# Performance work log

Measured on AMD Instinct MI355X. Metric: run time of the kernel, lower is better.

Reference implementation:

```python
import jax, jax.numpy as jnp
import numpy as np

NEG_SLOPE = 0.01  # torch F.leaky_relu default


def _gcn(x, W, b, src, dst, w, n_nodes):
    # PyG GCNConv(normalize=False, add_self_loops=False):
    # out[i] = sum_{e:(j->i)} w_e * (x @ W)[j] + b
    xw = x @ W                              # [N, out]
    msg = w[:, None] * xw[src]              # [E, out] gather
    return jax.ops.segment_sum(msg, dst, num_segments=n_nodes) + b


def setup_inputs() -> dict:
    key = jax.random.key(0)
    ks = jax.random.split(key, 12)
    N, E, B = 50000, 800000, 50
    d_in, d_hid, d_out = 128, 128, 128
    nodes_per_graph = N // B

    features = jax.random.normal(ks[0], (N, d_in), dtype=jnp.float32)
    adjs = jax.random.randint(ks[1], (2, E), 0, N, dtype=jnp.int32)
    values = jax.random.uniform(ks[2], (E,), dtype=jnp.float32)
    # root of graph g is its first node
    root_idx = jnp.arange(B, dtype=jnp.int32) * nodes_per_graph
    knowledge_node_num = jnp.full((B,), nodes_per_graph, dtype=jnp.int32)
    knowledge_edge_num = jnp.full((B,), E // B, dtype=jnp.int32)
    batch = jnp.arange(N, dtype=jnp.int32) // nodes_per_graph

    scale = 1.0 / np.sqrt(d_in)
    W1 = jax.random.uniform(ks[3], (d_in, d_hid), jnp.float32, -scale, scale)
    b1 = jax.random.uniform(ks[4], (d_hid,), jnp.float32, -scale, scale)
    W2 = jax.random.uniform(ks[5], (d_hid + d_in, d_out), jnp.float32, -scale, scale)
    b2 = jax.random.uniform(ks[6], (d_out,), jnp.float32, -scale, scale)
    Wl = jax.random.uniform(ks[7], (d_out + d_hid, d_in), jnp.float32, -scale, scale)
    bl = jax.random.uniform(ks[8], (d_in,), jnp.float32, -scale, scale)

    return {"features": features, "values": values, "W1": W1, "b1": b1,
            "W2": W2, "b2": b2, "Wl": Wl, "bl": bl,
            "adjs": adjs, "root_idx": root_idx,
            "knowledge_node_num": knowledge_node_num,
            "knowledge_edge_num": knowledge_edge_num, "batch": batch}


def reference(features, values, W1, b1, W2, b2, Wl, bl,
              adjs, root_idx, knowledge_node_num, knowledge_edge_num, batch):
    N = features.shape[0]
    B = knowledge_node_num.shape[0]
    src, dst = adjs[0], adjs[1]

    # per-node graph id (replaces the python loop building batch_k)
    batch_k = jnp.repeat(jnp.arange(B), knowledge_node_num, total_repeat_length=N)

    x0 = features                                    # features_1
    h1 = _gcn(x0, W1, b1, src, dst, values, N)       # conv1; features_2

    # root_extend: each node gets the raw features of its graph's root
    root1 = x0[root_idx[batch_k]]                    # [N, d_in]
    h = jax.nn.leaky_relu(jnp.concatenate([h1, root1], axis=1), NEG_SLOPE)
    # dropout=0.0 -> identity

    h2 = jax.nn.leaky_relu(_gcn(h, W2, b2, src, dst, values, N), NEG_SLOPE)

    root2 = h1[root_idx[batch_k]]                    # [N, d_hid] from conv1 output
    h = jnp.concatenate([h2, root2], axis=1)
    out = jax.nn.leaky_relu(h @ Wl + bl, NEG_SLOPE)
    return out
```

## Files before the change

kernel.cpp:

```cpp
#include <hip/hip_runtime.h>
#include <hip/hip_bf16.h>

#define NEG_SLOPE 0.01f
#define SCAN_CHUNK 1024

typedef __attribute__((ext_vector_type(8))) short short8;
typedef __attribute__((ext_vector_type(4))) float f32x4;

__device__ __forceinline__ float lrelu(float x) { return x > 0.f ? x : NEG_SLOPE * x; }

__device__ __forceinline__ unsigned short f2bf(float f) {
    unsigned u = __builtin_bit_cast(unsigned, f);
    u += 0x7fffu + ((u >> 16) & 1u);
    return (unsigned short)(u >> 16);
}
__device__ __forceinline__ float bf2f(unsigned short h) {
    return __builtin_bit_cast(float, (unsigned)h << 16);
}
__device__ __forceinline__ float bflo(unsigned u) {
    return __builtin_bit_cast(float, u << 16);
}
__device__ __forceinline__ float bfhi(unsigned u) {
    return __builtin_bit_cast(float, u & 0xffff0000u);
}

__global__ __launch_bounds__(256) void prep_kernel(
        const float* __restrict__ features, const int* __restrict__ batch,
        const int* __restrict__ root_idx, const float* __restrict__ W1,
        const float* __restrict__ W2, const float* __restrict__ Wl,
        unsigned short* __restrict__ feat16, int* __restrict__ rmap,
        int* __restrict__ deg, unsigned short* __restrict__ wt1,
        unsigned short* __restrict__ wt2, unsigned short* __restrict__ wtl, int N) {
    const int total = N * 32;
    for (int i = blockIdx.x * blockDim.x + threadIdx.x; i < total;
         i += gridDim.x * blockDim.x) {
        float4 v = *(const float4*)(features + (size_t)i * 4);
        ushort4 p;
        p.x = f2bf(v.x); p.y = f2bf(v.y); p.z = f2bf(v.z); p.w = f2bf(v.w);
        *(ushort4*)(feat16 + (size_t)i * 4) = p;
        if (i < N) { rmap[i] = root_idx[batch[i]]; deg[i] = 0; }
        if (i < 128 * 128) {
            int k = i >> 7, c = i & 127;
            wt1[c * 128 + k] = f2bf(W1[i]);
        }
        if (i < 256 * 128) {
            int k = i >> 7, c = i & 127;
            wt2[c * 256 + k] = f2bf(W2[i]);
            wtl[c * 256 + k] = f2bf(Wl[i]);
        }
    }
}

__global__ void count_kernel(const int* __restrict__ dst, int* __restrict__ deg, int E) {
    const int stride = gridDim.x * blockDim.x;
    const int i = blockIdx.x * blockDim.x + threadIdx.x;
    const int e4 = E >> 2;
    for (int q = i; q < e4; q += stride) {
        int4 d = ((const int4*)dst)[q];
        atomicAdd(&deg[d.x], 1);
        atomicAdd(&deg[d.y], 1);
        atomicAdd(&deg[d.z], 1);
        atomicAdd(&deg[d.w], 1);
    }
    for (int e = e4 * 4 + i; e < E; e += stride) atomicAdd(&deg[dst[e]], 1);
}

__global__ __launch_bounds__(256) void scan1_kernel(const int* __restrict__ deg,
                                                    int* __restrict__ rowstart,
                                                    int* __restrict__ chunksum, int N) {
    __shared__ int ts[256];
    const int b = blockIdx.x, t = threadIdx.x;
    const int base = b * SCAN_CHUNK + t * 4;
    int v[4], s = 0;
#pragma unroll
    for (int j = 0; j < 4; ++j) {
        v[j] = (base + j < N) ? deg[base + j] : 0;
        s += v[j];
    }
    ts[t] = s;
    __syncthreads();
    for (int off = 1; off < 256; off <<= 1) {
        int x = (t >= off) ? ts[t - off] : 0;
        __syncthreads();
        ts[t] += x;
        __syncthreads();
    }
    int run = ts[t] - s;
#pragma unroll
    for (int j = 0; j < 4; ++j) {
        if (base + j < N) rowstart[base + j] = run;
        run += v[j];
    }
    if (t == 255) chunksum[b] = ts[255];
}

__global__ void scan2_kernel(const int* __restrict__ chunksum, int* __restrict__ chunkoff,
                             int nchunks, int* __restrict__ rowstart, int N, int E) {
    if (blockIdx.x == 0 && threadIdx.x == 0) {
        int acc = 0;
        for (int i = 0; i < nchunks; ++i) { chunkoff[i] = acc; acc += chunksum[i]; }
        rowstart[N] = E;
    }
}

__global__ void scan3_kernel(int* __restrict__ rowstart, const int* __restrict__ chunkoff,
                             int* __restrict__ cursor, int N) {
    for (int i = blockIdx.x * blockDim.x + threadIdx.x; i < N; i += gridDim.x * blockDim.x) {
        int v = rowstart[i] + chunkoff[i / SCAN_CHUNK];
        rowstart[i] = v;
        cursor[i] = v;
    }
}

__global__ void fill_kernel(const int* __restrict__ src, const int* __restrict__ dst,
                            const float* __restrict__ vals, int* __restrict__ cursor,
                            int2* __restrict__ edata, int E) {
    const int stride = gridDim.x * blockDim.x;
    const int i = blockIdx.x * blockDim.x + threadIdx.x;
    const int e4 = E >> 2;
    for (int q = i; q < e4; q += stride) {
        int4 s = ((const int4*)src)[q];
        int4 d = ((const int4*)dst)[q];
        float4 v = ((const float4*)vals)[q];
        int p;
        p = atomicAdd(&cursor[d.x], 1);
        edata[p] = make_int2(s.x, __builtin_bit_cast(int, v.x));
        p = atomicAdd(&cursor[d.y], 1);
        edata[p] = make_int2(s.y, __builtin_bit_cast(int, v.y));
        p = atomicAdd(&cursor[d.z], 1);
        edata[p] = make_int2(s.z, __builtin_bit_cast(int, v.z));
        p = atomicAdd(&cursor[d.w], 1);
        edata[p] = make_int2(s.w, __builtin_bit_cast(int, v.w));
    }
    for (int e = e4 * 4 + i; e < E; e += stride) {
        int p = atomicAdd(&cursor[dst[e]], 1);
        edata[p] = make_int2(src[e], __builtin_bit_cast(int, vals[e]));
    }
}

__global__ __launch_bounds__(256) void gather_kernel(const unsigned short* __restrict__ xw,
                                                     const int* __restrict__ rowstart,
                                                     const int2* __restrict__ edata,
                                                     const float* __restrict__ bias,
                                                     unsigned short* __restrict__ h, int N) {
    const int node = blockIdx.x * 4 + (threadIdx.x >> 6);
    const int lane = threadIdx.x & 63;
    if (node >= N) return;
    const int s0 = rowstart[node], s1 = rowstart[node + 1];
    float2 acc = *(const float2*)(bias + lane * 2);
    int e = s0;
    for (; e + 4 <= s1; e += 4) {
        int2 e0 = edata[e], e1 = edata[e + 1], e2 = edata[e + 2], e3 = edata[e + 3];
        unsigned xa = *(const unsigned*)(xw + (size_t)e0.x * 128 + lane * 2);
        unsigned xb = *(const unsigned*)(xw + (size_t)e1.x * 128 + lane * 2);
        unsigned xc = *(const unsigned*)(xw + (size_t)e2.x * 128 + lane * 2);
        unsigned xd = *(const unsigned*)(xw + (size_t)e3.x * 128 + lane * 2);
        float va = __builtin_bit_cast(float, e0.y), vb = __builtin_bit_cast(float, e1.y);
        float vc = __builtin_bit_cast(float, e2.y), vd = __builtin_bit_cast(float, e3.y);
        acc.x = fmaf(va, bflo(xa), acc.x);
        acc.y = fmaf(va, bfhi(xa), acc.y);
        acc.x = fmaf(vb, bflo(xb), acc.x);
        acc.y = fmaf(vb, bfhi(xb), acc.y);
        acc.x = fmaf(vc, bflo(xc), acc.x);
        acc.y = fmaf(vc, bfhi(xc), acc.y);
        acc.x = fmaf(vd, bflo(xd), acc.x);
        acc.y = fmaf(vd, bfhi(xd), acc.y);
    }
    for (; e < s1; ++e) {
        int2 e0 = edata[e];
        float va = __builtin_bit_cast(float, e0.y);
        unsigned xa = *(const unsigned*)(xw + (size_t)e0.x * 128 + lane * 2);
        acc.x = fmaf(va, bflo(xa), acc.x);
        acc.y = fmaf(va, bfhi(xa), acc.y);
    }
    unsigned pk = (unsigned)f2bf(acc.x) | ((unsigned)f2bf(acc.y) << 16);
    *(unsigned*)(h + (size_t)node * 128 + lane * 2) = pk;
}

template <int K, bool LRA, bool LRB, bool LROUT, bool HASB, bool OUTBF>
__global__ __launch_bounds__(256) void mgemm_kernel(const unsigned short* __restrict__ A,
                                                    const unsigned short* __restrict__ B2,
                                                    const int* __restrict__ rmap,
                                                    const unsigned short* __restrict__ Wt,
                                                    const float* __restrict__ bias,
                                                    void* __restrict__ outv, int N) {
    __shared__ short As[64 * 32];
    __shared__ short Bs[128 * 32];
    const int tid = threadIdx.x;
    const int wv = tid >> 6, lane = tid & 63;
    const int lr = lane & 15, lg = lane >> 4;
    const int row0 = blockIdx.x * 64;

    const int arow = tid >> 2, apart = tid & 3;
    const int grow = row0 + arow;
    const int gr = grow < N ? grow : N - 1;
    const int rr = (K > 128) ? rmap[gr] : 0;
    const int bc = tid & 127, bhalf = (tid >> 7) * 16;

    f32x4 acc[8];
#pragma unroll
    for (int t = 0; t < 8; ++t) acc[t] = (f32x4){0.f, 0.f, 0.f, 0.f};

#pragma unroll 1
    for (int kc = 0; kc < K / 32; ++kc) {
        const int k0 = kc * 32;
        {
            const int kbase = k0 + apart * 8;
            const bool inA = kbase < 128;
            const unsigned short* sp = inA ? A + (size_t)gr * 128 + kbase
                                           : B2 + (size_t)rr * 128 + (kbase - 128);
            short8 v = *(const short8*)sp;
            const bool dolr = inA ? LRA : LRB;
            if (dolr) {
#pragma unroll
                for (int j = 0; j < 8; ++j)
                    v[j] = (short)f2bf(lrelu(bf2f((unsigned short)v[j])));
            }
            *(short8*)&As[arow * 32 + apart * 8] = v;
        }
        {
            const unsigned short* wsrc = Wt + (size_t)bc * K + k0 + bhalf;
            *(short8*)&Bs[bc * 32 + bhalf]     = *(const short8*)wsrc;
            *(short8*)&Bs[bc * 32 + bhalf + 8] = *(const short8*)(wsrc + 8);
        }
        __syncthreads();
        short8 af = *(short8*)&As[(wv * 16 + lr) * 32 + lg * 8];
#pragma unroll
        for (int t = 0; t < 8; ++t) {
            short8 bf = *(short8*)&Bs[(t * 16 + lr) * 32 + lg * 8];
            acc[t] = __builtin_amdgcn_mfma_f32_16x16x32_bf16(af, bf, acc[t], 0, 0, 0);
        }
        __syncthreads();
    }

#pragma unroll
    for (int t = 0; t < 8; ++t) {
#pragma unroll
        for (int r = 0; r < 4; ++r) {
            int grr = row0 + wv * 16 + lg * 4 + r;
            if (grr < N) {
                float v = acc[t][r];
                if (HASB) v += bias[t * 16 + lr];
                if (LROUT) v = lrelu(v);
                if (OUTBF)
                    ((unsigned short*)outv)[(size_t)grr * 128 + t * 16 + lr] = f2bf(v);
                else
                    ((float*)outv)[(size_t)grr * 128 + t * 16 + lr] = v;
            }
        }
    }
}

extern "C" void kernel_launch(void* const* d_in, const int* in_sizes, int n_in,
                              void* d_out, int out_size, void* d_ws, size_t ws_size,
                              hipStream_t stream) {
    const float* features = (const float*)d_in[0];
    const float* values   = (const float*)d_in[1];
    const float* W1 = (const float*)d_in[2];
    const float* b1 = (const float*)d_in[3];
    const float* W2 = (const float*)d_in[4];
    const float* b2 = (const float*)d_in[5];
    const float* Wl = (const float*)d_in[6];
    const float* bl = (const float*)d_in[7];
    const int* adjs     = (const int*)d_in[8];
    const int* root_idx = (const int*)d_in[9];
    const int* batch    = (const int*)d_in[12];
    float* out = (float*)d_out;

    const int N = in_sizes[0] / 128;
    const int E = in_sizes[1];
    const int* src = adjs;
    const int* dst = adjs + E;

    const size_t nf = (size_t)N * 128;
    unsigned short* bufA   = (unsigned short*)d_ws;
    unsigned short* h1     = bufA + nf;
    unsigned short* h2     = h1 + nf;
    unsigned short* feat16 = h2 + nf;
    unsigned short* wt1 = feat16 + nf;
    unsigned short* wt2 = wt1 + 128 * 128;
    unsigned short* wtl = wt2 + 256 * 128;
    uintptr_t ep = ((uintptr_t)(wtl + 256 * 128) + 7) & ~(uintptr_t)7;
    int2* edata    = (int2*)ep;
    int*  rmap     = (int*)(edata + E);
    int*  deg      = rmap + N;
    int*  rowstart = deg + N;
    int*  cursor   = rowstart + N + 1;
    int*  chunksum = cursor + N;
    int*  chunkoff = chunksum + 128;

    const int nchunks = (N + SCAN_CHUNK - 1) / SCAN_CHUNK;
    const int gblocks = (N + 63) / 64;

    prep_kernel<<<1024, 256, 0, stream>>>(features, batch, root_idx, W1, W2, Wl,
                                          feat16, rmap, deg, wt1, wt2, wtl, N);
    count_kernel<<<512, 256, 0, stream>>>(dst, deg, E);
    scan1_kernel<<<nchunks, 256, 0, stream>>>(deg, rowstart, chunksum, N);
    scan2_kernel<<<1, 64, 0, stream>>>(chunksum, chunkoff, nchunks, rowstart, N, E);
    scan3_kernel<<<64, 256, 0, stream>>>(rowstart, chunkoff, cursor, N);
    fill_kernel<<<512, 256, 0, stream>>>(src, dst, values, cursor, edata, E);

    mgemm_kernel<128, false, false, false, false, true>
        <<<gblocks, 256, 0, stream>>>(feat16, nullptr, nullptr, wt1, nullptr, bufA, N);
    gather_kernel<<<(N + 3) / 4, 256, 0, stream>>>(bufA, rowstart, edata, b1, h1, N);

    mgemm_kernel<256, true, true, false, false, true>
        <<<gblocks, 256, 0, stream>>>(h1, feat16, rmap, wt2, nullptr, bufA, N);
    gather_kernel<<<(N + 3) / 4, 256, 0, stream>>>(bufA, rowstart, edata, b2, h2, N);

    mgemm_kernel<256, true, false, true, true, false>
        <<<gblocks, 256, 0, stream>>>(h2, h1, rmap, wtl, bl, out, N);
}
```

Before: 311.6 us.

## Build CSR via two-level bucket sort with shared-memory histograms

Replaces global per-node atomic degree counting and atomic scatter with a two-pass bucketed sort: edges are first binned into 256-node buckets using block-local histograms and staging, then each bucket block computes node degrees and scatters locally in shared memory. This cuts random global atomics and the multi-kernel scan. It packs source index into 16 bits and limits buckets to 256, so it only works for N below 65536, and it adds an extra staging buffer pass.

```diff
diff --git a/kernel.cpp b/kernel.cpp
--- a/kernel.cpp
+++ b/kernel.cpp
@@ -2,7 +2,8 @@
 #include <hip/hip_bf16.h>
 
 #define NEG_SLOPE 0.01f
-#define SCAN_CHUNK 1024
+#define NBUK_MAX 256
+#define ATILE 2048
 
 typedef __attribute__((ext_vector_type(8))) short short8;
 typedef __attribute__((ext_vector_type(4))) float f32x4;
@@ -29,8 +30,9 @@
         const int* __restrict__ root_idx, const float* __restrict__ W1,
         const float* __restrict__ W2, const float* __restrict__ Wl,
         unsigned short* __restrict__ feat16, int* __restrict__ rmap,
-        int* __restrict__ deg, unsigned short* __restrict__ wt1,
-        unsigned short* __restrict__ wt2, unsigned short* __restrict__ wtl, int N) {
+        int* __restrict__ bucket_count, unsigned short* __restrict__ wt1,
+        unsigned short* __restrict__ wt2, unsigned short* __restrict__ wtl,
+        int N, int nbuk) {
     const int total = N * 32;
     for (int i = blockIdx.x * blockDim.x + threadIdx.x; i < total;
          i += gridDim.x * blockDim.x) {
@@ -38,7 +40,8 @@
         ushort4 p;
         p.x = f2bf(v.x); p.y = f2bf(v.y); p.z = f2bf(v.z); p.w = f2bf(v.w);
         *(ushort4*)(feat16 + (size_t)i * 4) = p;
-        if (i < N) { rmap[i] = root_idx[batch[i]]; deg[i] = 0; }
+        if (i < N) rmap[i] = root_idx[batch[i]];
+        if (i < nbuk) bucket_count[i] = 0;
         if (i < 128 * 128) {
             int k = i >> 7, c = i & 127;
             wt1[c * 128 + k] = f2bf(W1[i]);
@@ -51,90 +54,148 @@
     }
 }
 
-__global__ void count_kernel(const int* __restrict__ dst, int* __restrict__ deg, int E) {
-    const int stride = gridDim.x * blockDim.x;
-    const int i = blockIdx.x * blockDim.x + threadIdx.x;
-    const int e4 = E >> 2;
-    for (int q = i; q < e4; q += stride) {
-        int4 d = ((const int4*)dst)[q];
-        atomicAdd(&deg[d.x], 1);
-        atomicAdd(&deg[d.y], 1);
-        atomicAdd(&deg[d.z], 1);
-        atomicAdd(&deg[d.w], 1);
-    }
-    for (int e = e4 * 4 + i; e < E; e += stride) atomicAdd(&deg[dst[e]], 1);
-}
-
-__global__ __launch_bounds__(256) void scan1_kernel(const int* __restrict__ deg,
+__global__ __launch_bounds__(256) void histA_kernel(const int* __restrict__ dst,
+                                                    int* __restrict__ bucket_count,
+                                                    int E, int nbuk) {
+    __shared__ int hist[NBUK_MAX];
+    if (threadIdx.x < nbuk) hist[threadIdx.x] = 0;
+    __syncthreads();
+    for (int e = blockIdx.x * blockDim.x + threadIdx.x; e < E; e += gridDim.x * blockDim.x)
+        atomicAdd(&hist[dst[e] >> 8], 1);
+    __syncthreads();
+    if (threadIdx.x < nbuk) {
+        int v = hist[threadIdx.x];
+        if (v) atomicAdd(&bucket_count[threadIdx.x], v);
+    }
+}
+
+__global__ __launch_bounds__(256) void scanA_kernel(const int* __restrict__ bucket_count,
+                                                    int* __restrict__ bucket_base,
+                                                    int* __restrict__ bucket_cursor,
                                                     int* __restrict__ rowstart,
-                                                    int* __restrict__ chunksum, int N) {
-    __shared__ int ts[256];
-    const int b = blockIdx.x, t = threadIdx.x;
-    const int base = b * SCAN_CHUNK + t * 4;
-    int v[4], s = 0;
-#pragma unroll
-    for (int j = 0; j < 4; ++j) {
-        v[j] = (base + j < N) ? deg[base + j] : 0;
-        s += v[j];
-    }
-    ts[t] = s;
+                                                    int N, int E, int nbuk) {
+    __shared__ int sb[256];
+    const int t = threadIdx.x;
+    int v = (t < nbuk) ? bucket_count[t] : 0;
+    sb[t] = v;
     __syncthreads();
     for (int off = 1; off < 256; off <<= 1) {
-        int x = (t >= off) ? ts[t - off] : 0;
-        __syncthreads();
-        ts[t] += x;
-        __syncthreads();
-    }
-    int run = ts[t] - s;
-#pragma unroll
-    for (int j = 0; j < 4; ++j) {
-        if (base + j < N) rowstart[base + j] = run;
-        run += v[j];
-    }
-    if (t == 255) chunksum[b] = ts[255];
-}
-
-__global__ void scan2_kernel(const int* __restrict__ chunksum, int* __restrict__ chunkoff,
-                             int nchunks, int* __restrict__ rowstart, int N, int E) {
-    if (blockIdx.x == 0 && threadIdx.x == 0) {
-        int acc = 0;
-        for (int i = 0; i < nchunks; ++i) { chunkoff[i] = acc; acc += chunksum[i]; }
+        int x = (t >= off) ? sb[t - off] : 0;
+        __syncthreads();
+        sb[t] += x;
+        __syncthreads();
+    }
+    if (t < nbuk) {
+        int ex = sb[t] - v;
+        bucket_base[t] = ex;
+        bucket_cursor[t] = ex;
+    }
+    if (t == 0) {
+        bucket_base[nbuk] = sb[255];
         rowstart[N] = E;
     }
 }
 
-__global__ void scan3_kernel(int* __restrict__ rowstart, const int* __restrict__ chunkoff,
-                             int* __restrict__ cursor, int N) {
-    for (int i = blockIdx.x * blockDim.x + threadIdx.x; i < N; i += gridDim.x * blockDim.x) {
-        int v = rowstart[i] + chunkoff[i / SCAN_CHUNK];
-        rowstart[i] = v;
-        cursor[i] = v;
-    }
-}
-
-__global__ void fill_kernel(const int* __restrict__ src, const int* __restrict__ dst,
-                            const float* __restrict__ vals, int* __restrict__ cursor,
-                            int2* __restrict__ edata, int E) {
-    const int stride = gridDim.x * blockDim.x;
-    const int i = blockIdx.x * blockDim.x + threadIdx.x;
-    const int e4 = E >> 2;
-    for (int q = i; q < e4; q += stride) {
-        int4 s = ((const int4*)src)[q];
-        int4 d = ((const int4*)dst)[q];
-        float4 v = ((const float4*)vals)[q];
-        int p;
-        p = atomicAdd(&cursor[d.x], 1);
-        edata[p] = make_int2(s.x, __builtin_bit_cast(int, v.x));
-        p = atomicAdd(&cursor[d.y], 1);
-        edata[p] = make_int2(s.y, __builtin_bit_cast(int, v.y));
-        p = atomicAdd(&cursor[d.z], 1);
-        edata[p] = make_int2(s.z, __builtin_bit_cast(int, v.z));
-        p = atomicAdd(&cursor[d.w], 1);
-        edata[p] = make_int2(s.w, __builtin_bit_cast(int, v.w));
-    }
-    for (int e = e4 * 4 + i; e < E; e += stride) {
-        int p = atomicAdd(&cursor[dst[e]], 1);
-        edata[p] = make_int2(src[e], __builtin_bit_cast(int, vals[e]));
+__global__ __launch_bounds__(256) void binA_kernel(const int* __restrict__ src,
+                                                   const int* __restrict__ dst,
+                                                   const float* __restrict__ vals,
+                                                   int* __restrict__ bucket_cursor,
+                                                   int2* __restrict__ bstage,
+                                                   int E, int nbuk) {
+    __shared__ int hist[NBUK_MAX];
+    __shared__ int lbase[NBUK_MAX + 1];
+    __shared__ int gbase[NBUK_MAX];
+    __shared__ int cur[NBUK_MAX];
+    __shared__ int scanbuf[256];
+    __shared__ int2 stage[ATILE];
+    const int tid = threadIdx.x;
+    const int t0 = blockIdx.x * ATILE;
+    const int cnt = min(ATILE, E - t0);
+
+    if (tid < nbuk) hist[tid] = 0;
+    __syncthreads();
+
+    int s8[8], d8[8], v8[8];
+#pragma unroll
+    for (int k = 0; k < 8; ++k) {
+        const int li = k * 256 + tid;
+        const bool ok = li < cnt;
+        const int idx = t0 + li;
+        s8[k] = ok ? src[idx] : 0;
+        d8[k] = ok ? dst[idx] : 0;
+        v8[k] = ok ? ((const int*)vals)[idx] : 0;
+        if (ok) atomicAdd(&hist[d8[k] >> 8], 1);
+    }
+    __syncthreads();
+    const int h = (tid < nbuk) ? hist[tid] : 0;
+    scanbuf[tid] = h;
+    __syncthreads();
+    for (int off = 1; off < 256; off <<= 1) {
+        int x = (tid >= off) ? scanbuf[tid - off] : 0;
+        __syncthreads();
+        scanbuf[tid] += x;
+        __syncthreads();
+    }
+    if (tid < nbuk) {
+        const int ex = scanbuf[tid] - h;
+        lbase[tid] = ex;
+        cur[tid] = ex;
+        gbase[tid] = h ? atomicAdd(&bucket_cursor[tid], h) : 0;
+    }
+    if (tid == 0) lbase[nbuk] = cnt;
+    __syncthreads();
+#pragma unroll
+    for (int k = 0; k < 8; ++k) {
+        if ((k * 256 + tid) < cnt) {
+            const int b = d8[k] >> 8;
+            const int lp = atomicAdd(&cur[b], 1);
+            stage[lp] = make_int2((s8[k] & 0xffff) | ((d8[k] & 255) << 16), v8[k]);
+        }
+    }
+    __syncthreads();
+    for (int i = tid; i < cnt; i += 256) {
+        int lo = 0, hi = nbuk;
+        while (hi - lo > 1) {
+            const int mid = (lo + hi) >> 1;
+            if (lbase[mid] <= i) lo = mid; else hi = mid;
+        }
+        bstage[gbase[lo] + (i - lbase[lo])] = stage[i];
+    }
+}
+
+__global__ __launch_bounds__(256) void binB_kernel(const int2* __restrict__ bstage,
+                                                   const int* __restrict__ bucket_base,
+                                                   int* __restrict__ rowstart,
+                                                   int2* __restrict__ edata, int N) {
+    __shared__ int deg_l[256];
+    __shared__ int pfx[256];
+    const int b = blockIdx.x;
+    const int base = bucket_base[b], end = bucket_base[b + 1];
+    const int n0 = b << 8;
+    const int tid = threadIdx.x;
+    deg_l[tid] = 0;
+    __syncthreads();
+    for (int i = base + tid; i < end; i += 256)
+        atomicAdd(&deg_l[(bstage[i].x >> 16) & 255], 1);
+    __syncthreads();
+    const int v = deg_l[tid];
+    pfx[tid] = v;
+    __syncthreads();
+    for (int off = 1; off < 256; off <<= 1) {
+        int x = (tid >= off) ? pfx[tid - off] : 0;
+        __syncthreads();
+        pfx[tid] += x;
+        __syncthreads();
+    }
+    const int ex = pfx[tid] - v;
+    if (n0 + tid < N) rowstart[n0 + tid] = base + ex;
+    __syncthreads();
+    deg_l[tid] = ex;
+    __syncthreads();
+    for (int i = base + tid; i < end; i += 256) {
+        const int2 r = bstage[i];
+        const int lp = atomicAdd(&deg_l[(r.x >> 16) & 255], 1);
+        edata[base + lp] = make_int2(r.x & 0xffff, r.y);
     }
 }
 
@@ -271,6 +332,7 @@
     const int E = in_sizes[1];
     const int* src = adjs;
     const int* dst = adjs + E;
+    const int nbuk = (N + 255) >> 8;
 
     const size_t nf = (size_t)N * 128;
     unsigned short* bufA   = (unsigned short*)d_ws;
@@ -281,24 +343,25 @@
     unsigned short* wt2 = wt1 + 128 * 128;
     unsigned short* wtl = wt2 + 256 * 128;
     uintptr_t ep = ((uintptr_t)(wtl + 256 * 128) + 7) & ~(uintptr_t)7;
-    int2* edata    = (int2*)ep;
-    int*  rmap     = (int*)(edata + E);
-    int*  deg      = rmap + N;
-    int*  rowstart = deg + N;
-    int*  cursor   = rowstart + N + 1;
-    int*  chunksum = cursor + N;
-    int*  chunkoff = chunksum + 128;
-
-    const int nchunks = (N + SCAN_CHUNK - 1) / SCAN_CHUNK;
+    int2* edata  = (int2*)ep;
+    int2* bstage = edata + E;
+    int*  rmap     = (int*)(bstage + E);
+    int*  rowstart = rmap + N;
+    int*  bucket_count  = rowstart + N + 1;
+    int*  bucket_base   = bucket_count + NBUK_MAX;
+    int*  bucket_cursor = bucket_base + NBUK_MAX + 1;
+
     const int gblocks = (N + 63) / 64;
 
     prep_kernel<<<1024, 256, 0, stream>>>(features, batch, root_idx, W1, W2, Wl,
-                                          feat16, rmap, deg, wt1, wt2, wtl, N);
-    count_kernel<<<512, 256, 0, stream>>>(dst, deg, E);
-    scan1_kernel<<<nchunks, 256, 0, stream>>>(deg, rowstart, chunksum, N);
-    scan2_kernel<<<1, 64, 0, stream>>>(chunksum, chunkoff, nchunks, rowstart, N, E);
-    scan3_kernel<<<64, 256, 0, stream>>>(rowstart, chunkoff, cursor, N);
-    fill_kernel<<<512, 256, 0, stream>>>(src, dst, values, cursor, edata, E);
+                                          feat16, rmap, bucket_count, wt1, wt2, wtl,
+                                          N, nbuk);
+    histA_kernel<<<256, 256, 0, stream>>>(dst, bucket_count, E, nbuk);
+    scanA_kernel<<<1, 256, 0, stream>>>(bucket_count, bucket_base, bucket_cursor,
+                                        rowstart, N, E, nbuk);
+    binA_kernel<<<(E + ATILE - 1) / ATILE, 256, 0, stream>>>(src, dst, values,
+                                                             bucket_cursor, bstage, E, nbuk);
+    binB_kernel<<<nbuk, 256, 0, stream>>>(bstage, bucket_base, rowstart, edata, N);
 
     mgemm_kernel<128, false, false, false, false, true>
         <<<gblocks, 256, 0, stream>>>(feat16, nullptr, nullptr, wt1, nullptr, bufA, N);
```

Result: faster. 273.0 us (-12.4%).
